# Kernel tuning notes

Hardware: AMD Instinct MI355X
Metric: run time of the kernel (lower is better)

Reference implementation:

```python
import jax, jax.numpy as jnp
import numpy as np

N = 65536          # collocation points
NB = 32            # n_buses
H = 256            # hidden width (two hidden layers)
TMAX = 20.0        # t_max for input normalisation


def _glorot(k, shape):
    lim = np.sqrt(2.0 / (shape[0] + shape[1])).astype(np.float32)
    return jax.random.normal(k, shape, jnp.float32) * lim


def setup_inputs() -> dict:
    key = jax.random.key(0)
    ks = jax.random.split(key, 8)
    return {
        "input_time": jax.random.uniform(ks[0], (N, 1), jnp.float32) * TMAX,
        "input_power": jax.random.normal(ks[1], (N, NB), jnp.float32),
        "W0": _glorot(ks[2], (1, H)),   "b0": jnp.zeros((H,), jnp.float32),
        "W1": _glorot(ks[3], (H, H)),   "b1": jnp.zeros((H,), jnp.float32),
        "W2": _glorot(ks[4], (H, NB)),  "b2": jnp.zeros((NB,), jnp.float32),
        "lambda_m": jnp.ones((1, NB), jnp.float32),
        "lambda_d": jnp.ones((1, NB), jnp.float32),
        "lambda_b": jax.random.uniform(ks[5], (NB, NB), jnp.float32),
        "bus_with_inertia": jnp.ones((1, NB), jnp.float32),
    }


def reference(input_time, input_power, W0, b0, W1, b1, W2, b2,
              lambda_m, lambda_d, lambda_b, bus_with_inertia):
    def mlp(t):  # scalar time -> [NB] angles
        x = 2.0 * t / TMAX - 1.0          # NormaliseInputLayer (t_min = 0)
        h = jnp.tanh(x * W0[0] + b0)      # [H]
        h = jnp.tanh(h @ W1 + b1)         # [H]
        return h @ W2 + b2                # [NB]

    one = jnp.float32(1.0)

    def f_and_dt(t):
        return jax.jvp(mlp, (t,), (one,))  # (delta, d delta/dt)

    def all3(t):
        (out, out_t), (_, out_tt) = jax.jvp(f_and_dt, (t,), (one,))
        return out, out_t, out_tt

    # vectorize the nested forward-mode derivatives over all samples at once
    out, out_t, out_tt = jax.vmap(all3)(input_time[:, 0])  # each [N, NB]

    # pairwise sin coupling: sum_j B_ij * sin(delta_i - delta_j)
    diff = out[:, :, None] - out[:, None, :]               # [N, NB, NB]
    connectivity = jnp.sum(lambda_b * jnp.sin(diff), axis=2)  # [N, NB]

    physics = (lambda_m * bus_with_inertia * out_tt
               + lambda_d * out_t
               + connectivity - input_power)

    return out, out_t, physics
```

## Files before the change

kernel.cpp:

```cpp
#include <hip/hip_runtime.h>

#define NPTS 65536
#define NB 32
#define H 256
#define K2E 2.8853900817779268f

typedef __attribute__((ext_vector_type(8))) short bhalf8;
typedef __attribute__((ext_vector_type(4))) float f32x4;

union BHU { bhalf8 h; uint u[4]; };

__device__ __forceinline__ float bf2f(ushort u) {
  union { uint x; float f; } c; c.x = ((uint)u) << 16; return c.f;
}
__device__ __forceinline__ ushort f2bf(float f) {
  uint x = __float_as_uint(f);
  uint r = x + 0x7FFFu + ((x >> 16) & 1u);
  return (ushort)(r >> 16);
}
__device__ __forceinline__ uint packrne(float a, float b) {
  return (uint)f2bf(a) | ((uint)f2bf(b) << 16);
}
__device__ __forceinline__ ushort trunc1(float f) {
  return (ushort)(__float_as_uint(f) >> 16);
}
__device__ __forceinline__ uint packtr(float a, float b) {
  return (__float_as_uint(a) >> 16) | (__float_as_uint(b) & 0xFFFF0000u);
}
__device__ __forceinline__ float tanh_pf(float z2e) {
  float e = exp2f(z2e);
  float r = __builtin_amdgcn_rcpf(e + 1.0f);
  return fmaf(-2.0f, r, 1.0f);
}

__device__ __forceinline__ bool detect_bf16(const void* W1) {
  const uint4* p = (const uint4*)W1;
  int cnt = 0;
#pragma unroll
  for (int i = 0; i < 8; i++) {
    uint4 v = p[i];
    uint d[4] = {v.x, v.y, v.z, v.w};
#pragma unroll
    for (int k = 0; k < 4; k++) {
      int e = (d[k] >> 7) & 0xFF;
      cnt += (e >= 0x70 && e <= 0x7E) ? 1 : 0;
    }
  }
  return cnt >= 16;
}

template<bool B16> __device__ __forceinline__ float LD(const void* p, int i) {
  if constexpr (B16) return bf2f(((const ushort*)p)[i]);
  else               return ((const float*)p)[i];
}
template<bool B16> __device__ __forceinline__ void ST(void* p, int i, float v) {
  if constexpr (B16) ((ushort*)p)[i] = f2bf(v);
  else               ((float*)p)[i] = v;
}

__global__ void swz_kernel(const void* W1, const void* W2,
                           ushort* __restrict__ W1s, ushort* __restrict__ W2s) {
  int gid = blockIdx.x * 256 + threadIdx.x;
  bool b16 = detect_bf16(W1);
  if (gid < 65536) {
    int r = gid & 15, q = (gid >> 4) & 3, j = (gid >> 6) & 7;
    int kk = (gid >> 9) & 7, ct = gid >> 12;
    int src = (kk * 32 + q * 8 + j) * H + ct * 16 + r;
    int dst = ((ct * 8 + kk) * 64 + q * 16 + r) * 8 + j;
    float v = b16 ? bf2f(((const ushort*)W1)[src]) : ((const float*)W1)[src];
    W1s[dst] = f2bf(v);
  } else {
    int g2 = gid - 65536;
    int r = g2 & 15, q = (g2 >> 4) & 3, j = (g2 >> 6) & 7;
    int kk = (g2 >> 9) & 7, ct = (g2 >> 12) & 1;
    int src = (kk * 32 + q * 8 + j) * NB + ct * 16 + r;
    int dst = ((ct * 8 + kk) * 64 + q * 16 + r) * 8 + j;
    float v = b16 ? bf2f(((const ushort*)W2)[src]) : ((const float*)W2)[src];
    W2s[dst] = f2bf(v);
  }
}

#define PPITCH 40

struct Smem {
  alignas(16) ushort pairw[4][48 * PPITCH];
  alignas(16) ushort W2l[16 * 64 * 8];
  alignas(16) ushort lamTf[2 * 64 * 8];
  alignas(16) float  w0c[H], w0e[H], b0e[H], b1e[H];
  alignas(16) float  b2c[NB], lamMc[NB], lamDc[NB];
};

template<bool B16>
__device__ void pinn_body(Smem& sm,
                          const void* timeP, const void* powerP,
                          const void* W0, const void* b0,
                          const void* b1, const void* b2,
                          const void* lam_m, const void* lam_d,
                          const void* lam_b, const void* bwi,
                          const ushort* __restrict__ W1s, void* outP) {
  const int tid = threadIdx.x;
  const int wave = tid >> 6, lane = tid & 63;
  const int q = lane >> 4, r = lane & 15;

#pragma unroll
  for (int i = 0; i < 4; i++) {
    int c = tid + i * 256;
    *(bhalf8*)(sm.W2l + c * 8) = *(const bhalf8*)(((const ushort*)W1s) + H * H + c * 8);
  }
  if (tid < 128) {
    int ct = tid >> 6, l2 = tid & 63, qq = l2 >> 4, rr = l2 & 15;
    BHU t;
#pragma unroll
    for (int j = 0; j < 8; j += 2)
      t.u[j >> 1] = packrne(LD<B16>(lam_b, (ct * 16 + rr) * NB + qq * 8 + j),
                            LD<B16>(lam_b, (ct * 16 + rr) * NB + qq * 8 + j + 1));
    *(bhalf8*)(sm.lamTf + tid * 8) = t.h;
  }
  if (tid < H) {
    float w0v = LD<B16>(W0, tid);
    sm.w0c[tid] = w0v;
    sm.w0e[tid] = K2E * w0v;
    sm.b0e[tid] = K2E * LD<B16>(b0, tid);
    sm.b1e[tid] = K2E * LD<B16>(b1, tid);
  }
  if (tid < NB) {
    sm.b2c[tid]   = LD<B16>(b2, tid);
    sm.lamMc[tid] = LD<B16>(lam_m, tid) * LD<B16>(bwi, tid);
    sm.lamDc[tid] = LD<B16>(lam_d, tid);
  }
  __syncthreads();

  const int s0 = (blockIdx.x * 4 + wave) * 16;
  ushort* pw = &sm.pairw[wave][0];

  float t = LD<B16>(timeP, s0 + r);
  float x = t * 0.1f - 1.0f;

  bhalf8 a0f[8], a1f[8], a2f[8];
#pragma unroll
  for (int kk = 0; kk < 8; kk++) {
    int k0 = kk * 32 + q * 8;
    float4 wA = *(const float4*)&sm.w0c[k0];
    float4 wB = *(const float4*)&sm.w0c[k0 + 4];
    float4 eA = *(const float4*)&sm.w0e[k0];
    float4 eB = *(const float4*)&sm.w0e[k0 + 4];
    float4 bA = *(const float4*)&sm.b0e[k0];
    float4 bB = *(const float4*)&sm.b0e[k0 + 4];
    float w0v[8] = {wA.x, wA.y, wA.z, wA.w, wB.x, wB.y, wB.z, wB.w};
    float w0ev[8] = {eA.x, eA.y, eA.z, eA.w, eB.x, eB.y, eB.z, eB.w};
    float b0ev[8] = {bA.x, bA.y, bA.z, bA.w, bB.x, bB.y, bB.z, bB.w};
    BHU t0, t1, t2;
    float vv[8], d1v[8], d2v[8];
#pragma unroll
    for (int j = 0; j < 8; j++) {
      float v = tanh_pf(fmaf(x, w0ev[j], b0ev[j]));
      float cc = w0v[j] * 0.1f;
      float s2 = 1.0f - v * v;
      vv[j] = v; d1v[j] = s2 * cc; d2v[j] = -2.0f * v * d1v[j] * cc;
    }
#pragma unroll
    for (int j = 0; j < 8; j += 2) {
      t0.u[j >> 1] = packtr(vv[j], vv[j + 1]);
      t1.u[j >> 1] = packtr(d1v[j], d1v[j + 1]);
      t2.u[j >> 1] = packtr(d2v[j], d2v[j + 1]);
    }
    a0f[kk] = t0.h; a1f[kk] = t1.h; a2f[kk] = t2.h;
  }

  f32x4 acc2[3][2];
#pragma unroll
  for (int ch = 0; ch < 3; ch++)
#pragma unroll
    for (int c2 = 0; c2 < 2; c2++) { f32x4 z = {0.f,0.f,0.f,0.f}; acc2[ch][c2] = z; }

  bhalf8 bfA[8], bfB[8];
#pragma unroll
  for (int kk = 0; kk < 8; kk++)
    bfA[kk] = *(const bhalf8*)(W1s + ((0 * 8 + kk) * 64 + lane) * 8);

#pragma unroll 1
  for (int p = 0; p < 8; p++) {
    const int ct0 = 2 * p, ct1 = 2 * p + 1;

#pragma unroll
    for (int kk = 0; kk < 8; kk++)
      bfB[kk] = *(const bhalf8*)(W1s + ((ct1 * 8 + kk) * 64 + lane) * 8);

    f32x4 c0 = {0.f,0.f,0.f,0.f}, c1 = c0, c2 = c0;
#pragma unroll
    for (int kk = 0; kk < 8; kk++) {
      c0 = __builtin_amdgcn_mfma_f32_16x16x32_bf16(a0f[kk], bfA[kk], c0, 0, 0, 0);
      c1 = __builtin_amdgcn_mfma_f32_16x16x32_bf16(a1f[kk], bfA[kk], c1, 0, 0, 0);
      c2 = __builtin_amdgcn_mfma_f32_16x16x32_bf16(a2f[kk], bfA[kk], c2, 0, 0, 0);
    }

    if (p >= 1) {
      bhalf8 hf0 = *(const bhalf8*)(pw + (0 * 16 + r) * PPITCH + q * 8);
      bhalf8 hf1 = *(const bhalf8*)(pw + (1 * 16 + r) * PPITCH + q * 8);
      bhalf8 hf2 = *(const bhalf8*)(pw + (2 * 16 + r) * PPITCH + q * 8);
#pragma unroll
      for (int c2i = 0; c2i < 2; c2i++) {
        bhalf8 w2f = *(const bhalf8*)(sm.W2l + ((c2i * 8 + (p - 1)) * 64 + lane) * 8);
        acc2[0][c2i] = __builtin_amdgcn_mfma_f32_16x16x32_bf16(hf0, w2f, acc2[0][c2i], 0, 0, 0);
        acc2[1][c2i] = __builtin_amdgcn_mfma_f32_16x16x32_bf16(hf1, w2f, acc2[1][c2i], 0, 0, 0);
        acc2[2][c2i] = __builtin_amdgcn_mfma_f32_16x16x32_bf16(hf2, w2f, acc2[2][c2i], 0, 0, 0);
      }
    }

    {
      float b1v = sm.b1e[ct0 * 16 + r];
#pragma unroll
      for (int i = 0; i < 4; i++) {
        float hv  = tanh_pf(fmaf(c0[i], K2E, b1v));
        float s2  = 1.0f - hv * hv;
        float hd  = s2 * c1[i];
        float hdd = s2 * c2[i] - 2.0f * hv * hd * c1[i];
        int row = q * 4 + i;
        pw[row * PPITCH + r]        = trunc1(hv);
        pw[(16 + row) * PPITCH + r] = trunc1(hd);
        pw[(32 + row) * PPITCH + r] = trunc1(hdd);
      }
    }

    if (p < 7) {
#pragma unroll
      for (int kk = 0; kk < 8; kk++)
        bfA[kk] = *(const bhalf8*)(W1s + (((ct0 + 2) * 8 + kk) * 64 + lane) * 8);
    }

    {
      f32x4 d0 = {0.f,0.f,0.f,0.f}, d1 = d0, d2 = d0;
#pragma unroll
      for (int kk = 0; kk < 8; kk++) {
        d0 = __builtin_amdgcn_mfma_f32_16x16x32_bf16(a0f[kk], bfB[kk], d0, 0, 0, 0);
        d1 = __builtin_amdgcn_mfma_f32_16x16x32_bf16(a1f[kk], bfB[kk], d1, 0, 0, 0);
        d2 = __builtin_amdgcn_mfma_f32_16x16x32_bf16(a2f[kk], bfB[kk], d2, 0, 0, 0);
      }
      float b1v = sm.b1e[ct1 * 16 + r];
      int lc = 16 + r;
#pragma unroll
      for (int i = 0; i < 4; i++) {
        float hv  = tanh_pf(fmaf(d0[i], K2E, b1v));
        float s2  = 1.0f - hv * hv;
        float hd  = s2 * d1[i];
        float hdd = s2 * d2[i] - 2.0f * hv * hd * d1[i];
        int row = q * 4 + i;
        pw[row * PPITCH + lc]        = trunc1(hv);
        pw[(16 + row) * PPITCH + lc] = trunc1(hd);
        pw[(32 + row) * PPITCH + lc] = trunc1(hdd);
      }
    }
  }
  {
    bhalf8 hf0 = *(const bhalf8*)(pw + (0 * 16 + r) * PPITCH + q * 8);
    bhalf8 hf1 = *(const bhalf8*)(pw + (1 * 16 + r) * PPITCH + q * 8);
    bhalf8 hf2 = *(const bhalf8*)(pw + (2 * 16 + r) * PPITCH + q * 8);
#pragma unroll
    for (int c2i = 0; c2i < 2; c2i++) {
      bhalf8 w2f = *(const bhalf8*)(sm.W2l + ((c2i * 8 + 7) * 64 + lane) * 8);
      acc2[0][c2i] = __builtin_amdgcn_mfma_f32_16x16x32_bf16(hf0, w2f, acc2[0][c2i], 0, 0, 0);
      acc2[1][c2i] = __builtin_amdgcn_mfma_f32_16x16x32_bf16(hf1, w2f, acc2[1][c2i], 0, 0, 0);
      acc2[2][c2i] = __builtin_amdgcn_mfma_f32_16x16x32_bf16(hf2, w2f, acc2[2][c2i], 0, 0, 0);
    }
  }

  float dv[2][4], dt[2][4], dtt[2][4], sn[2][4], cs[2][4], Pv[2][4];
#pragma unroll
  for (int c2 = 0; c2 < 2; c2++) {
    int b = c2 * 16 + r;
    float b2v = sm.b2c[b];
#pragma unroll
    for (int i = 0; i < 4; i++) {
      int n = s0 + q * 4 + i;
      Pv[c2][i] = LD<B16>(powerP, n * NB + b);
      dv[c2][i]  = acc2[0][c2][i] + b2v;
      dt[c2][i]  = acc2[1][c2][i];
      dtt[c2][i] = acc2[2][c2][i];
      __sincosf(dv[c2][i], &sn[c2][i], &cs[c2][i]);
      pw[(q * 4 + i) * PPITCH + b]        = trunc1(sn[c2][i]);
      pw[(16 + q * 4 + i) * PPITCH + b]   = trunc1(cs[c2][i]);
      ST<B16>(outP, n * NB + b, dv[c2][i]);
      ST<B16>(outP, NPTS * NB + n * NB + b, dt[c2][i]);
    }
  }
  bhalf8 snA = *(const bhalf8*)(pw + r * PPITCH + q * 8);
  bhalf8 csA = *(const bhalf8*)(pw + (16 + r) * PPITCH + q * 8);
  f32x4 accC[2], accS[2];
#pragma unroll
  for (int c2 = 0; c2 < 2; c2++) {
    bhalf8 lt = *(const bhalf8*)(sm.lamTf + (c2 * 64 + lane) * 8);
    f32x4 z = {0.f,0.f,0.f,0.f};
    accC[c2] = __builtin_amdgcn_mfma_f32_16x16x32_bf16(csA, lt, z, 0, 0, 0);
    accS[c2] = __builtin_amdgcn_mfma_f32_16x16x32_bf16(snA, lt, z, 0, 0, 0);
  }
#pragma unroll
  for (int c2 = 0; c2 < 2; c2++) {
    int b = c2 * 16 + r;
    float lm = sm.lamMc[b], ld = sm.lamDc[b];
#pragma unroll
    for (int i = 0; i < 4; i++) {
      float conn = sn[c2][i] * accC[c2][i] - cs[c2][i] * accS[c2][i];
      float phys = lm * dtt[c2][i] + ld * dt[c2][i] + conn - Pv[c2][i];
      int n = s0 + q * 4 + i;
      ST<B16>(outP, 2 * NPTS * NB + n * NB + b, phys);
    }
  }
}

__global__ __launch_bounds__(256, 2)
void pinn_kernel(const void* timeP, const void* powerP,
                 const void* W0, const void* b0,
                 const void* b1, const void* b2,
                 const void* lam_m, const void* lam_d,
                 const void* lam_b, const void* bwi,
                 const void* W1_for_detect,
                 const ushort* __restrict__ W1s, void* outP) {
  __shared__ Smem sm;
  if (detect_bf16(W1_for_detect))
    pinn_body<true>(sm, timeP, powerP, W0, b0, b1, b2, lam_m, lam_d, lam_b, bwi,
                    W1s, outP);
  else
    pinn_body<false>(sm, timeP, powerP, W0, b0, b1, b2, lam_m, lam_d, lam_b, bwi,
                     W1s, outP);
}

extern "C" void kernel_launch(void* const* d_in, const int* in_sizes, int n_in,
                              void* d_out, int out_size, void* d_ws, size_t ws_size,
                              hipStream_t stream) {
  const void* timeP  = d_in[0];
  const void* powerP = d_in[1];
  const void* W0     = d_in[2];
  const void* b0     = d_in[3];
  const void* W1     = d_in[4];
  const void* b1     = d_in[5];
  const void* W2     = d_in[6];
  const void* b2     = d_in[7];
  const void* lam_m  = d_in[8];
  const void* lam_d  = d_in[9];
  const void* lam_b  = d_in[10];
  const void* bwi    = d_in[11];

  ushort* W1s = (ushort*)d_ws;
  ushort* W2s = W1s + H * H;

  swz_kernel<<<288, 256, 0, stream>>>(W1, W2, W1s, W2s);
  pinn_kernel<<<1024, 256, 0, stream>>>(timeP, powerP, W0, b0, b1, b2,
                                        lam_m, lam_d, lam_b, bwi, W1,
                                        W1s, d_out);
  (void)W2s;
}
```

Baseline: 122.6 us.

## Stage W1 tiles into LDS via async global_load_lds triple buffering

Each W1 column tile is now copied from global memory into a three-slot LDS ring with asynchronous global-to-LDS loads, so the next tiles are fetched while the current tile's MFMAs run, instead of holding two tiles of B fragments in registers. W2 fragments are read from global one iteration ahead in registers rather than staged in LDS. The change also raises occupancy to three blocks per SIMD via launch bounds, raises wave priority around the MFMA bursts, and precomputes the 0.1 scale on W0. Costs are the added barriers per half-iteration, the hand-written vmcnt waits that must match the number of outstanding loads, and tighter register limits.

```diff
diff --git a/kernel.cpp b/kernel.cpp
--- a/kernel.cpp
+++ b/kernel.cpp
@@ -84,11 +84,59 @@
 
 struct Smem {
   alignas(16) ushort pairw[4][48 * PPITCH];
-  alignas(16) ushort W2l[16 * 64 * 8];
+  alignas(16) ushort w1st[3][4096];
   alignas(16) ushort lamTf[2 * 64 * 8];
-  alignas(16) float  w0c[H], w0e[H], b0e[H], b1e[H];
+  alignas(16) float  w0d[H], w0e[H], b0e[H], b1e[H];
   alignas(16) float  b2c[NB], lamMc[NB], lamDc[NB];
 };
+
+__device__ __forceinline__ void stage_ct(const ushort* __restrict__ W1s,
+                                         ushort* buf, int ct, int wave, int lane) {
+#pragma unroll
+  for (int c = 0; c < 2; c++) {
+    const ushort* src = W1s + ct * 4096 + (wave * 2 + c) * 512 + lane * 8;
+    ushort* dst = buf + (wave * 2 + c) * 512;
+    __builtin_amdgcn_global_load_lds(
+        (const __attribute__((address_space(1))) unsigned int*)src,
+        (__attribute__((address_space(3))) unsigned int*)dst, 16, 0, 0);
+  }
+}
+
+__device__ __forceinline__ void gemm1(const ushort* __restrict__ buf, int lane,
+                                      const bhalf8* a0f, const bhalf8* a1f,
+                                      const bhalf8* a2f,
+                                      f32x4& c0, f32x4& c1, f32x4& c2) {
+  f32x4 z = {0.f, 0.f, 0.f, 0.f};
+  c0 = z; c1 = z; c2 = z;
+  bhalf8 bf[8];
+#pragma unroll
+  for (int kk = 0; kk < 8; kk++)
+    bf[kk] = *(const bhalf8*)(buf + (kk * 64 + lane) * 8);
+  __builtin_amdgcn_s_setprio(1);
+#pragma unroll
+  for (int kk = 0; kk < 8; kk++) {
+    c0 = __builtin_amdgcn_mfma_f32_16x16x32_bf16(a0f[kk], bf[kk], c0, 0, 0, 0);
+    c1 = __builtin_amdgcn_mfma_f32_16x16x32_bf16(a1f[kk], bf[kk], c1, 0, 0, 0);
+    c2 = __builtin_amdgcn_mfma_f32_16x16x32_bf16(a2f[kk], bf[kk], c2, 0, 0, 0);
+  }
+  __builtin_amdgcn_s_setprio(0);
+}
+
+__device__ __forceinline__ void chain(ushort* pw, float b1v, int q, int lc,
+                                      const f32x4& c0, const f32x4& c1,
+                                      const f32x4& c2) {
+#pragma unroll
+  for (int i = 0; i < 4; i++) {
+    float hv  = tanh_pf(fmaf(c0[i], K2E, b1v));
+    float s2  = 1.0f - hv * hv;
+    float hd  = s2 * c1[i];
+    float hdd = s2 * c2[i] - 2.0f * hv * hd * c1[i];
+    int row = q * 4 + i;
+    pw[row * PPITCH + lc]        = trunc1(hv);
+    pw[(16 + row) * PPITCH + lc] = trunc1(hd);
+    pw[(32 + row) * PPITCH + lc] = trunc1(hdd);
+  }
+}
 
 template<bool B16>
 __device__ void pinn_body(Smem& sm,
@@ -101,12 +149,11 @@
   const int tid = threadIdx.x;
   const int wave = tid >> 6, lane = tid & 63;
   const int q = lane >> 4, r = lane & 15;
-
-#pragma unroll
-  for (int i = 0; i < 4; i++) {
-    int c = tid + i * 256;
-    *(bhalf8*)(sm.W2l + c * 8) = *(const bhalf8*)(((const ushort*)W1s) + H * H + c * 8);
-  }
+  const ushort* W2s = W1s + H * H;
+
+  stage_ct(W1s, &sm.w1st[0][0], 0, wave, lane);
+  stage_ct(W1s, &sm.w1st[1][0], 1, wave, lane);
+
   if (tid < 128) {
     int ct = tid >> 6, l2 = tid & 63, qq = l2 >> 4, rr = l2 & 15;
     BHU t;
@@ -118,7 +165,7 @@
   }
   if (tid < H) {
     float w0v = LD<B16>(W0, tid);
-    sm.w0c[tid] = w0v;
+    sm.w0d[tid] = 0.1f * w0v;
     sm.w0e[tid] = K2E * w0v;
     sm.b0e[tid] = K2E * LD<B16>(b0, tid);
     sm.b1e[tid] = K2E * LD<B16>(b1, tid);
@@ -140,13 +187,13 @@
 #pragma unroll
   for (int kk = 0; kk < 8; kk++) {
     int k0 = kk * 32 + q * 8;
-    float4 wA = *(const float4*)&sm.w0c[k0];
-    float4 wB = *(const float4*)&sm.w0c[k0 + 4];
+    float4 wA = *(const float4*)&sm.w0d[k0];
+    float4 wB = *(const float4*)&sm.w0d[k0 + 4];
     float4 eA = *(const float4*)&sm.w0e[k0];
     float4 eB = *(const float4*)&sm.w0e[k0 + 4];
     float4 bA = *(const float4*)&sm.b0e[k0];
     float4 bB = *(const float4*)&sm.b0e[k0 + 4];
-    float w0v[8] = {wA.x, wA.y, wA.z, wA.w, wB.x, wB.y, wB.z, wB.w};
+    float w0dv[8] = {wA.x, wA.y, wA.z, wA.w, wB.x, wB.y, wB.z, wB.w};
     float w0ev[8] = {eA.x, eA.y, eA.z, eA.w, eB.x, eB.y, eB.z, eB.w};
     float b0ev[8] = {bA.x, bA.y, bA.z, bA.w, bB.x, bB.y, bB.z, bB.w};
     BHU t0, t1, t2;
@@ -154,7 +201,7 @@
 #pragma unroll
     for (int j = 0; j < 8; j++) {
       float v = tanh_pf(fmaf(x, w0ev[j], b0ev[j]));
-      float cc = w0v[j] * 0.1f;
+      float cc = w0dv[j];
       float s2 = 1.0f - v * v;
       vv[j] = v; d1v[j] = s2 * cc; d2v[j] = -2.0f * v * d1v[j] * cc;
     }
@@ -173,95 +220,64 @@
 #pragma unroll
     for (int c2 = 0; c2 < 2; c2++) { f32x4 z = {0.f,0.f,0.f,0.f}; acc2[ch][c2] = z; }
 
-  bhalf8 bfA[8], bfB[8];
-#pragma unroll
-  for (int kk = 0; kk < 8; kk++)
-    bfA[kk] = *(const bhalf8*)(W1s + ((0 * 8 + kk) * 64 + lane) * 8);
+  bhalf8 w2n0 = {}, w2n1 = {}, w2c0, w2c1;
+  int bcur = 0;
 
 #pragma unroll 1
-  for (int p = 0; p < 8; p++) {
+  for (int p = 0; p < 8; ++p) {
     const int ct0 = 2 * p, ct1 = 2 * p + 1;
-
-#pragma unroll
-    for (int kk = 0; kk < 8; kk++)
-      bfB[kk] = *(const bhalf8*)(W1s + ((ct1 * 8 + kk) * 64 + lane) * 8);
-
-    f32x4 c0 = {0.f,0.f,0.f,0.f}, c1 = c0, c2 = c0;
-#pragma unroll
-    for (int kk = 0; kk < 8; kk++) {
-      c0 = __builtin_amdgcn_mfma_f32_16x16x32_bf16(a0f[kk], bfA[kk], c0, 0, 0, 0);
-      c1 = __builtin_amdgcn_mfma_f32_16x16x32_bf16(a1f[kk], bfA[kk], c1, 0, 0, 0);
-      c2 = __builtin_amdgcn_mfma_f32_16x16x32_bf16(a2f[kk], bfA[kk], c2, 0, 0, 0);
-    }
+    int bn1 = bcur + 1; if (bn1 >= 3) bn1 -= 3;
+    int bn2 = bn1 + 1;  if (bn2 >= 3) bn2 -= 3;
+    ushort* bufA = &sm.w1st[bcur][0];
+    ushort* bufB = &sm.w1st[bn1][0];
+    ushort* bufC = &sm.w1st[bn2][0];
+
+    asm volatile("s_waitcnt vmcnt(2)\n\ts_barrier" ::: "memory");
+
+    w2c0 = w2n0; w2c1 = w2n1;
+    w2n0 = *(const bhalf8*)(W2s + ((0 * 8 + p) * 64 + lane) * 8);
+    w2n1 = *(const bhalf8*)(W2s + ((1 * 8 + p) * 64 + lane) * 8);
+
+    f32x4 c0, c1, c2;
+    gemm1(bufA, lane, a0f, a1f, a2f, c0, c1, c2);
+
+    if (p < 7) stage_ct(W1s, bufC, ct0 + 2, wave, lane);
 
     if (p >= 1) {
       bhalf8 hf0 = *(const bhalf8*)(pw + (0 * 16 + r) * PPITCH + q * 8);
       bhalf8 hf1 = *(const bhalf8*)(pw + (1 * 16 + r) * PPITCH + q * 8);
       bhalf8 hf2 = *(const bhalf8*)(pw + (2 * 16 + r) * PPITCH + q * 8);
-#pragma unroll
-      for (int c2i = 0; c2i < 2; c2i++) {
-        bhalf8 w2f = *(const bhalf8*)(sm.W2l + ((c2i * 8 + (p - 1)) * 64 + lane) * 8);
-        acc2[0][c2i] = __builtin_amdgcn_mfma_f32_16x16x32_bf16(hf0, w2f, acc2[0][c2i], 0, 0, 0);
-        acc2[1][c2i] = __builtin_amdgcn_mfma_f32_16x16x32_bf16(hf1, w2f, acc2[1][c2i], 0, 0, 0);
-        acc2[2][c2i] = __builtin_amdgcn_mfma_f32_16x16x32_bf16(hf2, w2f, acc2[2][c2i], 0, 0, 0);
-      }
-    }
-
-    {
-      float b1v = sm.b1e[ct0 * 16 + r];
-#pragma unroll
-      for (int i = 0; i < 4; i++) {
-        float hv  = tanh_pf(fmaf(c0[i], K2E, b1v));
-        float s2  = 1.0f - hv * hv;
-        float hd  = s2 * c1[i];
-        float hdd = s2 * c2[i] - 2.0f * hv * hd * c1[i];
-        int row = q * 4 + i;
-        pw[row * PPITCH + r]        = trunc1(hv);
-        pw[(16 + row) * PPITCH + r] = trunc1(hd);
-        pw[(32 + row) * PPITCH + r] = trunc1(hdd);
-      }
-    }
-
-    if (p < 7) {
-#pragma unroll
-      for (int kk = 0; kk < 8; kk++)
-        bfA[kk] = *(const bhalf8*)(W1s + (((ct0 + 2) * 8 + kk) * 64 + lane) * 8);
-    }
-
-    {
-      f32x4 d0 = {0.f,0.f,0.f,0.f}, d1 = d0, d2 = d0;
-#pragma unroll
-      for (int kk = 0; kk < 8; kk++) {
-        d0 = __builtin_amdgcn_mfma_f32_16x16x32_bf16(a0f[kk], bfB[kk], d0, 0, 0, 0);
-        d1 = __builtin_amdgcn_mfma_f32_16x16x32_bf16(a1f[kk], bfB[kk], d1, 0, 0, 0);
-        d2 = __builtin_amdgcn_mfma_f32_16x16x32_bf16(a2f[kk], bfB[kk], d2, 0, 0, 0);
-      }
-      float b1v = sm.b1e[ct1 * 16 + r];
-      int lc = 16 + r;
-#pragma unroll
-      for (int i = 0; i < 4; i++) {
-        float hv  = tanh_pf(fmaf(d0[i], K2E, b1v));
-        float s2  = 1.0f - hv * hv;
-        float hd  = s2 * d1[i];
-        float hdd = s2 * d2[i] - 2.0f * hv * hd * d1[i];
-        int row = q * 4 + i;
-        pw[row * PPITCH + lc]        = trunc1(hv);
-        pw[(16 + row) * PPITCH + lc] = trunc1(hd);
-        pw[(32 + row) * PPITCH + lc] = trunc1(hdd);
-      }
-    }
+      acc2[0][0] = __builtin_amdgcn_mfma_f32_16x16x32_bf16(hf0, w2c0, acc2[0][0], 0, 0, 0);
+      acc2[1][0] = __builtin_amdgcn_mfma_f32_16x16x32_bf16(hf1, w2c0, acc2[1][0], 0, 0, 0);
+      acc2[2][0] = __builtin_amdgcn_mfma_f32_16x16x32_bf16(hf2, w2c0, acc2[2][0], 0, 0, 0);
+      acc2[0][1] = __builtin_amdgcn_mfma_f32_16x16x32_bf16(hf0, w2c1, acc2[0][1], 0, 0, 0);
+      acc2[1][1] = __builtin_amdgcn_mfma_f32_16x16x32_bf16(hf1, w2c1, acc2[1][1], 0, 0, 0);
+      acc2[2][1] = __builtin_amdgcn_mfma_f32_16x16x32_bf16(hf2, w2c1, acc2[2][1], 0, 0, 0);
+    }
+
+    chain(pw, sm.b1e[ct0 * 16 + r], q, r, c0, c1, c2);
+
+    asm volatile("s_waitcnt vmcnt(2)\n\ts_barrier" ::: "memory");
+
+    f32x4 d0, d1, d2;
+    gemm1(bufB, lane, a0f, a1f, a2f, d0, d1, d2);
+
+    if (p < 7) stage_ct(W1s, bufA, ct1 + 2, wave, lane);
+
+    chain(pw, sm.b1e[ct1 * 16 + r], q, 16 + r, d0, d1, d2);
+
+    bcur = bn2;
   }
   {
     bhalf8 hf0 = *(const bhalf8*)(pw + (0 * 16 + r) * PPITCH + q * 8);
     bhalf8 hf1 = *(const bhalf8*)(pw + (1 * 16 + r) * PPITCH + q * 8);
     bhalf8 hf2 = *(const bhalf8*)(pw + (2 * 16 + r) * PPITCH + q * 8);
-#pragma unroll
-    for (int c2i = 0; c2i < 2; c2i++) {
-      bhalf8 w2f = *(const bhalf8*)(sm.W2l + ((c2i * 8 + 7) * 64 + lane) * 8);
-      acc2[0][c2i] = __builtin_amdgcn_mfma_f32_16x16x32_bf16(hf0, w2f, acc2[0][c2i], 0, 0, 0);
-      acc2[1][c2i] = __builtin_amdgcn_mfma_f32_16x16x32_bf16(hf1, w2f, acc2[1][c2i], 0, 0, 0);
-      acc2[2][c2i] = __builtin_amdgcn_mfma_f32_16x16x32_bf16(hf2, w2f, acc2[2][c2i], 0, 0, 0);
-    }
+    acc2[0][0] = __builtin_amdgcn_mfma_f32_16x16x32_bf16(hf0, w2n0, acc2[0][0], 0, 0, 0);
+    acc2[1][0] = __builtin_amdgcn_mfma_f32_16x16x32_bf16(hf1, w2n0, acc2[1][0], 0, 0, 0);
+    acc2[2][0] = __builtin_amdgcn_mfma_f32_16x16x32_bf16(hf2, w2n0, acc2[2][0], 0, 0, 0);
+    acc2[0][1] = __builtin_amdgcn_mfma_f32_16x16x32_bf16(hf0, w2n1, acc2[0][1], 0, 0, 0);
+    acc2[1][1] = __builtin_amdgcn_mfma_f32_16x16x32_bf16(hf1, w2n1, acc2[1][1], 0, 0, 0);
+    acc2[2][1] = __builtin_amdgcn_mfma_f32_16x16x32_bf16(hf2, w2n1, acc2[2][1], 0, 0, 0);
   }
 
   float dv[2][4], dt[2][4], dtt[2][4], sn[2][4], cs[2][4], Pv[2][4];
@@ -307,7 +323,7 @@
   }
 }
 
-__global__ __launch_bounds__(256, 2)
+__global__ __launch_bounds__(256, 3)
 void pinn_kernel(const void* timeP, const void* powerP,
                  const void* W0, const void* b0,
                  const void* b1, const void* b2,
```

Result: slower. 199.8 us (+62.9%).
